# Performance work log

Measured on AMD Instinct MI355X. Metric: run time of the kernel, lower is better.

The kernel has to match this reference:

```python
import jax, jax.numpy as jnp
import numpy as np

GROUPS = 32
EPS = 1e-5

def group_norm(x, scale, bias):
    b, c, h, w = x.shape
    xg = x.reshape(b, GROUPS, c // GROUPS, h, w)
    mean = xg.mean(axis=(2, 3, 4), keepdims=True)
    var = xg.var(axis=(2, 3, 4), keepdims=True)
    xg = (xg - mean) * jax.lax.rsqrt(var + EPS)
    x = xg.reshape(b, c, h, w)
    return x * scale[None, :, None, None] + bias[None, :, None, None]

def conv2d(x, w, b, pad):
    y = jax.lax.conv_general_dilated(
        x, w, window_strides=(1, 1), padding=[(pad, pad), (pad, pad)],
        dimension_numbers=('NCHW', 'OIHW', 'NCHW'))
    return y + b[None, :, None, None]

def setup_inputs() -> dict:
    key = jax.random.key(0)
    ks = jax.random.split(key, 16)
    B, Cin, Cout, H, W, TDIM, NCON = 4, 128, 128, 64, 64, 512, 4
    s = 0.05
    return {
        'x': jax.random.normal(ks[0], (B, Cin, H, W), jnp.float32),
        't': jax.random.normal(ks[1], (B, TDIM), jnp.float32),
        'aim': jax.random.randint(ks[2], (B,), 0, NCON),
        'cond': jax.random.normal(ks[3], (B, Cin, H, W), jnp.float32),
        'gn1_scale': jnp.ones((Cin,), jnp.float32),
        'gn1_bias': jnp.zeros((Cin,), jnp.float32),
        'conv1_w': jax.random.normal(ks[4], (Cout, Cin, 3, 3), jnp.float32) * s,
        'conv1_b': jnp.zeros((Cout,), jnp.float32),
        'mlp_w': jax.random.normal(ks[5], (Cout, TDIM), jnp.float32) * s,
        'mlp_b': jnp.zeros((Cout,), jnp.float32),
        'cond_w': jax.random.normal(ks[6], (Cout, Cin, 1, 1), jnp.float32) * s,
        'cond_b': jnp.zeros((Cout,), jnp.float32),
        'gn2_scale': jnp.ones((Cout,), jnp.float32),
        'gn2_bias': jnp.zeros((Cout,), jnp.float32),
        'conv2_w': jax.random.normal(ks[7], (Cout, Cout, 3, 3), jnp.float32) * s,
        'conv2_b': jnp.zeros((Cout,), jnp.float32),
        'contrast_embed': jax.random.normal(ks[8], (NCON, Cout, 1, 1), jnp.float32),
    }

def reference(x, t, aim, cond, gn1_scale, gn1_bias, conv1_w, conv1_b,
              mlp_w, mlp_b, cond_w, cond_b, gn2_scale, gn2_bias,
              conv2_w, conv2_b, contrast_embed):
    # block1: GN -> SiLU -> 3x3 conv
    h = conv2d(jax.nn.silu(group_norm(x, gn1_scale, gn1_bias)), conv1_w, conv1_b, 1)
    # time embedding: SiLU -> Linear, broadcast over spatial
    temb = jax.nn.silu(t) @ mlp_w.T + mlp_b  # (b, out_ch)
    h = h + temb[:, :, None, None]
    # spatial cross-attention with cond
    c = conv2d(cond, cond_w, cond_b, 0)  # 1x1 projection, (b, C, u, v)
    C = h.shape[1]
    score = jnp.einsum('bchw,bcuv->bhwuv', h, c)  # (b, h, w, u, v)
    # NOTE: softmax over dim=1 (the spatial h axis), as in the source
    score = jax.nn.softmax(score / jnp.sqrt(jnp.float32(C)), axis=1)
    h = h + jnp.einsum('bhwuv,bcuv->bchw', score, c)
    # contrast embedding lookup
    h = h + contrast_embed[aim]  # (b, C, 1, 1) broadcast
    # block2: GN -> SiLU -> (dropout=identity at eval) -> 3x3 conv
    h = conv2d(jax.nn.silu(group_norm(h, gn2_scale, gn2_bias)), conv2_w, conv2_b, 1)
    # res_conv is Identity since in_ch == out_ch
    return h + x
```

## Files before the change

kernel.cpp:

```cpp
#include <hip/hip_runtime.h>
#include <cmath>

#define BB 4
#define CC 128
#define HH 64
#define WW 64
#define SP 4096
#define NG 32
#define TT 64
#define NS 2
#define PSZ ((size_t)BB * SP * CC)

typedef __bf16 bf16x8 __attribute__((ext_vector_type(8)));
typedef __bf16 bf16x4 __attribute__((ext_vector_type(4)));
typedef float  f32x4  __attribute__((ext_vector_type(4)));

__device__ __forceinline__ float silu_f(float v) {
    return v / (1.f + __expf(-v));
}

__device__ __forceinline__ float fast_exp2(float x) {
    return exp2f(x);
}

template<int CTRL>
__device__ __forceinline__ float dpp_add(float v) {
    int m = __builtin_amdgcn_update_dpp(0, __float_as_int(v), CTRL, 0xF, 0xF, true);
    return v + __int_as_float(m);
}
__device__ __forceinline__ float row16_sum(float v) {
    v = dpp_add<0xB1>(v);
    v = dpp_add<0x4E>(v);
    v = dpp_add<0x141>(v);
    v = dpp_add<0x140>(v);
    return v;
}

__global__ __launch_bounds__(256) void prep_kernel(
    const float* __restrict__ x, const float* __restrict__ gn1s,
    const float* __restrict__ gn1b, __bf16* __restrict__ aT,
    const float* __restrict__ c1w, const float* __restrict__ c2w,
    __bf16* __restrict__ wt,
    const float* __restrict__ t, const float* __restrict__ mlpw,
    const float* __restrict__ mlpb, float* __restrict__ tembw,
    const float* __restrict__ cond, const float* __restrict__ cw,
    const float* __restrict__ cb, __bf16* __restrict__ cmT,
    __bf16* __restrict__ cm2)
{
    __shared__ __align__(16) char pool[18432];
    __shared__ float rs[4], rs2[4], mean_s, inv_s;
    const int blk = blockIdx.x;
    const int tid = threadIdx.x;

    if (blk < 128) {
        const int b = blk >> 5, g = blk & 31;
        const float* p = x + (size_t)blk * 16384;
        float s = 0.f, s2 = 0.f;
        for (int it = 0; it < 16; ++it) {
            int q = it * 256 + tid;
            float4 v = *(const float4*)&p[q * 4];
            s += v.x + v.y + v.z + v.w;
            s2 += v.x * v.x + v.y * v.y + v.z * v.z + v.w * v.w;
        }
        #pragma unroll
        for (int off = 32; off >= 1; off >>= 1) {
            s  += __shfl_down(s,  off, 64);
            s2 += __shfl_down(s2, off, 64);
        }
        const int wid = tid >> 6;
        if ((tid & 63) == 0) { rs[wid] = s; rs2[wid] = s2; }
        __syncthreads();
        if (tid == 0) {
            float S = rs[0] + rs[1] + rs[2] + rs[3];
            float S2 = rs2[0] + rs2[1] + rs2[2] + rs2[3];
            float m = S * (1.f / 16384.f);
            float var = S2 * (1.f / 16384.f) - m * m;
            mean_s = m;
            inv_s = rsqrtf(var + 1e-5f);
        }
        __syncthreads();
        const float m = mean_s, inv = inv_s;
        float sc[4], bi[4];
        #pragma unroll
        for (int j = 0; j < 4; ++j) { sc[j] = gn1s[g * 4 + j]; bi[j] = gn1b[g * 4 + j]; }
        for (int it = 0; it < 16; ++it) {
            int pp = it * 256 + tid;
            bf16x4 o;
            #pragma unroll
            for (int j = 0; j < 4; ++j)
                o[j] = (__bf16)silu_f((p[j * 4096 + pp] - m) * inv * sc[j] + bi[j]);
            *(bf16x4*)&aT[((size_t)(b * SP + pp)) * CC + g * 4] = o;
        }
    } else if (blk < 146) {
        const int idx = blk - 128;
        const int wsel = idx / 9, tap = idx % 9;
        const float* src = wsel ? c2w : c1w;
        __bf16* dst = wt + (size_t)wsel * 9 * 16384 + (size_t)tap * 16384;
        for (int it = 0; it < 64; ++it) {
            int q = it * 256 + tid;
            dst[q] = (__bf16)src[(size_t)q * 9 + tap];
        }
    } else if (blk < 154) {
        const int cog = blk - 146;
        float* st = (float*)pool;
        for (int it = 0; it < 8; ++it) {
            int q = it * 256 + tid;
            st[q] = silu_f(t[q]);
        }
        __syncthreads();
        const int col = tid >> 4, seg = tid & 15;
        const float* wr = mlpw + (size_t)(cog * 16 + col) * 512 + seg * 32;
        float acc[4] = {0.f, 0.f, 0.f, 0.f};
        #pragma unroll
        for (int k8 = 0; k8 < 8; ++k8) {
            float4 wv = *(const float4*)&wr[k8 * 4];
            #pragma unroll
            for (int j = 0; j < 4; ++j) {
                int k = seg * 32 + k8 * 4 + j;
                float w4 = (&wv.x)[j];
                acc[0] += st[0 * 512 + k] * w4;
                acc[1] += st[1 * 512 + k] * w4;
                acc[2] += st[2 * 512 + k] * w4;
                acc[3] += st[3 * 512 + k] * w4;
            }
        }
        #pragma unroll
        for (int o = 1; o < 16; o <<= 1) {
            #pragma unroll
            for (int b4 = 0; b4 < 4; ++b4)
                acc[b4] += __shfl_xor(acc[b4], o, 64);
        }
        if (seg == 0) {
            float bv = mlpb[cog * 16 + col];
            #pragma unroll
            for (int b4 = 0; b4 < 4; ++b4)
                tembw[b4 * 128 + cog * 16 + col] = acc[b4] + bv;
        }
    } else {
        const int pblk = blk - 154;
        const int b = pblk >> 6;
        const int p0 = (pblk & 63) * 64;
        const int l = tid & 63, wv = tid >> 6;
        const int l15 = l & 15, l4 = l >> 4;
        const int mB = wv * 32;

        __bf16* XT = (__bf16*)pool;

        for (int it = 0; it < 32; ++it) {
            int q = it * 256 + tid;
            float v = cond[((size_t)(b * CC + (q >> 6))) * SP + p0 + (q & 63)];
            XT[(q & 63) * 136 + (q >> 6)] = (__bf16)v;
        }
        __syncthreads();

        f32x4 acc[2][4];
        #pragma unroll
        for (int mb = 0; mb < 2; ++mb)
            #pragma unroll
            for (int nt = 0; nt < 4; ++nt) acc[mb][nt] = (f32x4){0.f, 0.f, 0.f, 0.f};

        #pragma unroll
        for (int ks = 0; ks < 4; ++ks) {
            bf16x8 bfr[4];
            #pragma unroll
            for (int nt = 0; nt < 4; ++nt)
                bfr[nt] = *(const bf16x8*)&XT[(nt * 16 + l15) * 136 + ks * 32 + l4 * 8];
            #pragma unroll
            for (int mb = 0; mb < 2; ++mb) {
                const float* wrow = cw + (size_t)(mB + mb * 16 + l15) * 128 + ks * 32 + l4 * 8;
                float4 wa = *(const float4*)wrow;
                float4 wb4 = *(const float4*)(wrow + 4);
                bf16x8 afr;
                afr[0] = (__bf16)wa.x; afr[1] = (__bf16)wa.y;
                afr[2] = (__bf16)wa.z; afr[3] = (__bf16)wa.w;
                afr[4] = (__bf16)wb4.x; afr[5] = (__bf16)wb4.y;
                afr[6] = (__bf16)wb4.z; afr[7] = (__bf16)wb4.w;
                #pragma unroll
                for (int nt = 0; nt < 4; ++nt)
                    acc[mb][nt] = __builtin_amdgcn_mfma_f32_16x16x32_bf16(afr, bfr[nt], acc[mb][nt], 0, 0, 0);
            }
        }

        const float scl = 0.12751743f;
        #pragma unroll
        for (int mb = 0; mb < 2; ++mb) {
            int co0 = mB + mb * 16 + l4 * 4;
            float bv[4];
            #pragma unroll
            for (int r = 0; r < 4; ++r) bv[r] = cb[co0 + r];
            #pragma unroll
            for (int nt = 0; nt < 4; ++nt) {
                int p = p0 + nt * 16 + l15;
                bf16x4 o;
                #pragma unroll
                for (int r = 0; r < 4; ++r)
                    o[r] = (__bf16)((acc[mb][nt][r] + bv[r]) * scl);
                *(bf16x4*)&cmT[((size_t)(b * SP + p)) * CC + co0] = o;
            }
        }
        __syncthreads();
        __bf16* O2 = (__bf16*)pool;
        #pragma unroll
        for (int mb = 0; mb < 2; ++mb) {
            int co0 = mB + mb * 16 + l4 * 4;
            #pragma unroll
            for (int r = 0; r < 4; ++r) {
                float bv = cb[co0 + r];
                #pragma unroll
                for (int nt = 0; nt < 4; ++nt)
                    O2[(co0 + r) * 72 + nt * 16 + l15] = (__bf16)(acc[mb][nt][r] + bv);
            }
        }
        __syncthreads();
        #pragma unroll
        for (int it = 0; it < 4; ++it) {
            int q = it * 256 + tid;
            int co = q >> 3, pc = q & 7;
            *(bf16x8*)&cm2[((size_t)(b * CC + co)) * SP + p0 + pc * 8] =
                *(const bf16x8*)&O2[co * 72 + pc * 8];
        }
    }
}

template<bool FUSE_TEMB, bool OUT_CF, bool FUSE_GN>
__global__ __launch_bounds__(256, 4) void conv_mfma_kernel(
    const __bf16* __restrict__ inT, const __bf16* __restrict__ wt,
    const float* __restrict__ bias, const float* __restrict__ temb,
    const float* __restrict__ resid, __bf16* __restrict__ outT,
    float* __restrict__ outF, const float* __restrict__ gstat,
    const float* __restrict__ gn_s, const float* __restrict__ gn_b)
{
    const int y   = blockIdx.x >> 2;
    const int xh2 = (blockIdx.x >> 1) & 1;
    const int coh = blockIdx.x & 1;
    const int x0  = xh2 * 32;
    const int b   = blockIdx.y;
    const int tid = threadIdx.x;
    const int l = tid & 63, wv = tid >> 6;
    const int l15 = l & 15, l4 = l >> 4;
    const int co_w = coh * 64 + wv * 16;

    __shared__ __bf16 inS[3 * 16 * 34 * 8];
    __shared__ float af[128], bfp[128];

    if (FUSE_GN) {
        if (tid < 128) {
            int g = tid >> 2;
            float S = gstat[(b * NG + g) * 2], S2 = gstat[(b * NG + g) * 2 + 1];
            float m = S * (1.f / 16384.f);
            float var = S2 * (1.f / 16384.f) - m * m;
            float inv = rsqrtf(var + 1e-5f);
            float a = inv * gn_s[tid];
            af[tid] = a;
            bfp[tid] = gn_b[tid] - m * a;
        }
        __syncthreads();
    }

    const __bf16* inTb = inT + (size_t)b * SP * CC;
    for (int q = tid; q < 3 * 34 * 16; q += 256) {
        int cc = q & 15;
        int t2 = q >> 4;
        int xs = t2 % 34;
        int r  = t2 / 34;
        int yy = y + r - 1;
        int xg = x0 + xs - 1;
        bf16x8 v;
        if (((unsigned)yy < 64u) && ((unsigned)xg < 64u)) {
            bf16x8 raw = *(const bf16x8*)&inTb[((size_t)(yy * 64 + xg)) * CC + cc * 8];
            if (FUSE_GN) {
                #pragma unroll
                for (int j = 0; j < 8; ++j) {
                    int c = cc * 8 + j;
                    v[j] = (__bf16)silu_f((float)raw[j] * af[c] + bfp[c]);
                }
            } else {
                v = raw;
            }
        } else {
            #pragma unroll
            for (int j = 0; j < 8; ++j) v[j] = (__bf16)0.f;
        }
        *(bf16x8*)&inS[((r * 16 + cc) * 34 + xs) * 8] = v;
    }
    __syncthreads();

    f32x4 acc[2];
    acc[0] = (f32x4){0.f, 0.f, 0.f, 0.f};
    acc[1] = (f32x4){0.f, 0.f, 0.f, 0.f};

    const __bf16* wp = wt + (size_t)(co_w + l15) * 128 + l4 * 8;
    bf16x8 wb[2][4];
    #pragma unroll
    for (int ks = 0; ks < 4; ++ks)
        wb[0][ks] = *(const bf16x8*)(wp + ks * 32);

    #pragma unroll
    for (int tap = 0; tap < 9; ++tap) {
        const int cur = tap & 1, nxt = cur ^ 1;
        if (tap < 8) {
            #pragma unroll
            for (int ks = 0; ks < 4; ++ks)
                wb[nxt][ks] = *(const bf16x8*)(wp + (tap + 1) * 16384 + ks * 32);
        }
        const int rr = tap / 3, dx = tap % 3;
        #pragma unroll
        for (int ks = 0; ks < 4; ++ks) {
            const __bf16* rb = &inS[((rr * 16 + ks * 4 + l4) * 34) * 8];
            bf16x8 b0 = *(const bf16x8*)&rb[(dx + l15) * 8];
            bf16x8 b1 = *(const bf16x8*)&rb[(16 + dx + l15) * 8];
            acc[0] = __builtin_amdgcn_mfma_f32_16x16x32_bf16(wb[cur][ks], b0, acc[0], 0, 0, 0);
            acc[1] = __builtin_amdgcn_mfma_f32_16x16x32_bf16(wb[cur][ks], b1, acc[1], 0, 0, 0);
        }
    }

    if (OUT_CF) {
        #pragma unroll
        for (int r = 0; r < 4; ++r) {
            int co = co_w + l4 * 4 + r;
            float bv = bias[co];
            #pragma unroll
            for (int nb = 0; nb < 2; ++nb) {
                int p = y * 64 + x0 + nb * 16 + l15;
                size_t o = ((size_t)(b * CC + co)) * SP + p;
                outF[o] = acc[nb][r] + bv + resid[o];
            }
        }
    } else {
        int co0 = co_w + l4 * 4;
        float bv[4];
        #pragma unroll
        for (int r = 0; r < 4; ++r)
            bv[r] = bias[co0 + r] + (FUSE_TEMB ? temb[b * CC + co0 + r] : 0.f);
        #pragma unroll
        for (int nb = 0; nb < 2; ++nb) {
            int p = y * 64 + x0 + nb * 16 + l15;
            bf16x4 o;
            #pragma unroll
            for (int r = 0; r < 4; ++r)
                o[r] = (__bf16)(acc[nb][r] + bv[r]);
            *(bf16x4*)&outT[((size_t)(b * SP + p)) * CC + co0] = o;
        }
    }
}

#define CT2 72
#define PBS 72
#define POOL_BYTES 55296

__global__ __launch_bounds__(256, 2) void attn_kernel(
    const __bf16* __restrict__ h1T, const __bf16* __restrict__ cmT,
    const __bf16* __restrict__ cm2, __bf16* __restrict__ parts)
{
    const int w = blockIdx.x;
    const int b = blockIdx.y;
    const int s = blockIdx.z;
    const int tid = threadIdx.x;
    const int wl = tid >> 6;
    const int l = tid & 63, l15 = l & 15, l4 = l >> 4;
    const int hB = (wl & 1) * 32;
    const int cB = (wl >> 1) * 64;

    __shared__ __align__(16) char pool[POOL_BYTES];
    __bf16* ct2p = (__bf16*)pool;
    __bf16* Pbp  = (__bf16*)(pool + 36864);
    __bf16* Otr  = (__bf16*)pool;

    const __bf16* h1Tb = h1T + (size_t)b * SP * CC;
    const __bf16* cmTb = cmT + (size_t)b * SP * CC;
    const __bf16* cm2b = cm2 + (size_t)b * CC * SP;

    bf16x8 hfr[4][4];
    #pragma unroll
    for (int nt = 0; nt < 4; ++nt)
        #pragma unroll
        for (int ks = 0; ks < 4; ++ks)
            hfr[nt][ks] = *(const bf16x8*)&h1Tb[((size_t)((nt * 16 + l15) * WW + w)) * CC + ks * 32 + l4 * 8];

    f32x4 acc2[2][4];
    #pragma unroll
    for (int mb = 0; mb < 2; ++mb)
        #pragma unroll
        for (int nt = 0; nt < 4; ++nt) acc2[mb][nt] = (f32x4){0.f, 0.f, 0.f, 0.f};

    const int sc = tid >> 3;
    const int stc = tid & 7;

    {
        const int uv0 = s * TT;
        #pragma unroll
        for (int it = 0; it < 4; ++it) {
            int c = it * 32 + sc;
            *(bf16x8*)&ct2p[c * CT2 + stc * 8] =
                *(const bf16x8*)&cm2b[(size_t)c * SP + uv0 + stc * 8];
        }
        const __bf16* arow = cmTb + (size_t)(uv0 + 16 * wl + l15) * CC;
        bf16x8 afr[4];
        #pragma unroll
        for (int ks = 0; ks < 4; ++ks) afr[ks] = *(const bf16x8*)&arow[ks * 32 + l4 * 8];
        f32x4 s1[4];
        __builtin_amdgcn_s_setprio(1);
        #pragma unroll
        for (int nt = 0; nt < 4; ++nt) {
            s1[nt] = (f32x4){0.f, 0.f, 0.f, 0.f};
            #pragma unroll
            for (int ks = 0; ks < 4; ++ks)
                s1[nt] = __builtin_amdgcn_mfma_f32_16x16x32_bf16(afr[ks], hfr[nt][ks], s1[nt], 0, 0, 0);
        }
        __builtin_amdgcn_s_setprio(0);
        #pragma unroll
        for (int r = 0; r < 4; ++r) {
            float e0 = fast_exp2(s1[0][r]), e1 = fast_exp2(s1[1][r]);
            float e2 = fast_exp2(s1[2][r]), e3 = fast_exp2(s1[3][r]);
            float sm = (e0 + e1) + (e2 + e3);
            sm = row16_sum(sm);
            float ri = 1.f / sm;
            s1[0][r] = e0 * ri; s1[1][r] = e1 * ri;
            s1[2][r] = e2 * ri; s1[3][r] = e3 * ri;
        }
        #pragma unroll
        for (int nt = 0; nt < 4; ++nt) {
            bf16x4 pk;
            pk[0] = (__bf16)s1[nt][0]; pk[1] = (__bf16)s1[nt][1];
            pk[2] = (__bf16)s1[nt][2]; pk[3] = (__bf16)s1[nt][3];
            *(bf16x4*)&Pbp[(nt * 16 + l15) * PBS + 16 * wl + l4 * 4] = pk;
        }
    }

    for (int i = 0; i < SP / TT / NS; ++i) {
        const int cur = i & 1;
        __syncthreads();
        bf16x8 st4[4];
        bf16x8 afr[4];
        if (i < SP / TT / NS - 1) {
            const int uv0n = ((i + 1) * NS + s) * TT;
            #pragma unroll
            for (int it = 0; it < 4; ++it) {
                int c = it * 32 + sc;
                st4[it] = *(const bf16x8*)&cm2b[(size_t)c * SP + uv0n + stc * 8];
            }
            const __bf16* arow = cmTb + (size_t)(uv0n + 16 * wl + l15) * CC;
            #pragma unroll
            for (int ks = 0; ks < 4; ++ks) afr[ks] = *(const bf16x8*)&arow[ks * 32 + l4 * 8];
        }
        {
            const __bf16* PbR = Pbp + cur * 4608;
            const __bf16* ctR = ct2p + cur * 9216;
            bf16x8 pfr[2][2];
            #pragma unroll
            for (int mb = 0; mb < 2; ++mb)
                #pragma unroll
                for (int ks = 0; ks < 2; ++ks)
                    pfr[mb][ks] = *(const bf16x8*)&PbR[(hB + mb * 16 + l15) * PBS + ks * 32 + l4 * 8];
            bf16x8 bfr[4][2];
            #pragma unroll
            for (int nt = 0; nt < 4; ++nt)
                #pragma unroll
                for (int ks = 0; ks < 2; ++ks)
                    bfr[nt][ks] = *(const bf16x8*)&ctR[(cB + nt * 16 + l15) * CT2 + ks * 32 + l4 * 8];
            __builtin_amdgcn_s_setprio(1);
            #pragma unroll
            for (int mb = 0; mb < 2; ++mb)
                #pragma unroll
                for (int nt = 0; nt < 4; ++nt)
                    #pragma unroll
                    for (int ks = 0; ks < 2; ++ks)
                        acc2[mb][nt] = __builtin_amdgcn_mfma_f32_16x16x32_bf16(
                            pfr[mb][ks], bfr[nt][ks], acc2[mb][nt], 0, 0, 0);
            __builtin_amdgcn_s_setprio(0);
        }
        if (i < SP / TT / NS - 1) {
            __bf16* ctW = ct2p + (cur ^ 1) * 9216;
            #pragma unroll
            for (int it = 0; it < 4; ++it) {
                int c = it * 32 + sc;
                *(bf16x8*)&ctW[c * CT2 + stc * 8] = st4[it];
            }
            f32x4 s1[4];
            __builtin_amdgcn_s_setprio(1);
            #pragma unroll
            for (int nt = 0; nt < 4; ++nt) {
                s1[nt] = (f32x4){0.f, 0.f, 0.f, 0.f};
                #pragma unroll
                for (int ks = 0; ks < 4; ++ks)
                    s1[nt] = __builtin_amdgcn_mfma_f32_16x16x32_bf16(afr[ks], hfr[nt][ks], s1[nt], 0, 0, 0);
            }
            __builtin_amdgcn_s_setprio(0);
            #pragma unroll
            for (int r = 0; r < 4; ++r) {
                float e0 = fast_exp2(s1[0][r]), e1 = fast_exp2(s1[1][r]);
                float e2 = fast_exp2(s1[2][r]), e3 = fast_exp2(s1[3][r]);
                float sm = (e0 + e1) + (e2 + e3);
                sm = row16_sum(sm);
                float ri = 1.f / sm;
                s1[0][r] = e0 * ri; s1[1][r] = e1 * ri;
                s1[2][r] = e2 * ri; s1[3][r] = e3 * ri;
            }
            __bf16* PbW = Pbp + (cur ^ 1) * 4608;
            #pragma unroll
            for (int nt = 0; nt < 4; ++nt) {
                bf16x4 pk;
                pk[0] = (__bf16)s1[nt][0]; pk[1] = (__bf16)s1[nt][1];
                pk[2] = (__bf16)s1[nt][2]; pk[3] = (__bf16)s1[nt][3];
                *(bf16x4*)&PbW[(nt * 16 + l15) * PBS + 16 * wl + l4 * 4] = pk;
            }
        }
    }

    __syncthreads();
    #pragma unroll
    for (int mb = 0; mb < 2; ++mb)
        #pragma unroll
        for (int nt = 0; nt < 4; ++nt)
            #pragma unroll
            for (int r = 0; r < 4; ++r)
                Otr[(hB + mb * 16 + l4 * 4 + r) * 136 + cB + nt * 16 + l15] =
                    (__bf16)acc2[mb][nt][r];
    __syncthreads();
    __bf16* pO = parts + (size_t)s * PSZ;
    #pragma unroll
    for (int it = 0; it < 4; ++it) {
        int q = it * 256 + tid;
        int h = q >> 4, cc = q & 15;
        *(bf16x8*)&pO[((size_t)(b * SP + h * WW + w)) * CC + cc * 8] =
            *(const bf16x8*)&Otr[h * 136 + cc * 8];
    }
}

__global__ __launch_bounds__(256) void gn2_stats_kernel(
    const __bf16* __restrict__ h1T, const __bf16* __restrict__ parts,
    const int* __restrict__ aim, const float* __restrict__ emb,
    __bf16* __restrict__ h2T, float* __restrict__ gstat)
{
    const int pb = blockIdx.x, b = blockIdx.y;
    const int tid = threadIdx.x;
    const int c4 = tid & 31;
    const float4 ev = *(const float4*)&emb[aim[b] * CC + c4 * 4];
    float s = 0.f, s2 = 0.f;
    for (int it = 0; it < 8; ++it) {
        int prow = it * 8 + (tid >> 5);
        size_t base = ((size_t)(b * SP + pb * 64 + prow)) * CC + c4 * 4;
        bf16x4 hv = *(const bf16x4*)&h1T[base];
        float v0 = (float)hv[0] + ev.x;
        float v1 = (float)hv[1] + ev.y;
        float v2 = (float)hv[2] + ev.z;
        float v3 = (float)hv[3] + ev.w;
        #pragma unroll
        for (int k = 0; k < NS; ++k) {
            bf16x4 a = *(const bf16x4*)&parts[(size_t)k * PSZ + base];
            v0 += (float)a[0]; v1 += (float)a[1];
            v2 += (float)a[2]; v3 += (float)a[3];
        }
        bf16x4 o;
        o[0] = (__bf16)v0; o[1] = (__bf16)v1;
        o[2] = (__bf16)v2; o[3] = (__bf16)v3;
        *(bf16x4*)&h2T[base] = o;
        s += v0 + v1 + v2 + v3;
        s2 += v0 * v0 + v1 * v1 + v2 * v2 + v3 * v3;
    }
    s  += __shfl_down(s,  32, 64);
    s2 += __shfl_down(s2, 32, 64);
    __shared__ float ls[4][32][2];
    const int wv = tid >> 6, ll = tid & 63;
    if (ll < 32) { ls[wv][ll][0] = s; ls[wv][ll][1] = s2; }
    __syncthreads();
    if (tid < 32) {
        float S = ls[0][tid][0] + ls[1][tid][0] + ls[2][tid][0] + ls[3][tid][0];
        float S2 = ls[0][tid][1] + ls[1][tid][1] + ls[2][tid][1] + ls[3][tid][1];
        atomicAdd(&gstat[(b * NG + tid) * 2], S);
        atomicAdd(&gstat[(b * NG + tid) * 2 + 1], S2);
    }
}

extern "C" void kernel_launch(void* const* d_in, const int* in_sizes, int n_in,
                              void* d_out, int out_size, void* d_ws, size_t ws_size,
                              hipStream_t stream)
{
    const float* x     = (const float*)d_in[0];
    const float* t     = (const float*)d_in[1];
    const int*   aim   = (const int*)  d_in[2];
    const float* cond  = (const float*)d_in[3];
    const float* gn1s  = (const float*)d_in[4];
    const float* gn1b  = (const float*)d_in[5];
    const float* c1w   = (const float*)d_in[6];
    const float* c1b   = (const float*)d_in[7];
    const float* mlpw  = (const float*)d_in[8];
    const float* mlpb  = (const float*)d_in[9];
    const float* cw    = (const float*)d_in[10];
    const float* cb    = (const float*)d_in[11];
    const float* gn2s  = (const float*)d_in[12];
    const float* gn2b  = (const float*)d_in[13];
    const float* c2w   = (const float*)d_in[14];
    const float* c2b   = (const float*)d_in[15];
    const float* emb   = (const float*)d_in[16];
    float* out = (float*)d_out;
    float* ws = (float*)d_ws;

    __bf16* aT    = (__bf16*)ws;
    __bf16* h1T   = (__bf16*)(ws + 1048576);
    __bf16* cmT   = (__bf16*)(ws + 2097152);
    __bf16* cm2   = (__bf16*)(ws + 3145728);
    __bf16* parts = (__bf16*)(ws + 4194304);
    __bf16* wt    = (__bf16*)(ws + 6291456);
    float*  tembw = ws + 6438912;
    float*  gstat = ws + 6439424;
    __bf16* h2T   = cmT;

    prep_kernel<<<dim3(410), dim3(256), 0, stream>>>(
        x, gn1s, gn1b, aT, c1w, c2w, wt, t, mlpw, mlpb, tembw,
        cond, cw, cb, cmT, cm2);
    hipMemsetAsync(gstat, 0, 256 * sizeof(float), stream);
    conv_mfma_kernel<true, false, false><<<dim3(256, BB), dim3(256), 0, stream>>>(
        aT, wt, c1b, tembw, nullptr, h1T, nullptr, nullptr, nullptr, nullptr);
    attn_kernel<<<dim3(WW, BB, NS), dim3(256), 0, stream>>>(h1T, cmT, cm2, parts);
    gn2_stats_kernel<<<dim3(64, BB), dim3(256), 0, stream>>>(h1T, parts, aim, emb, h2T, gstat);
    conv_mfma_kernel<false, true, true><<<dim3(256, BB), dim3(256), 0, stream>>>(
        h2T, wt + (size_t)9 * 16384, c2b, nullptr, x, nullptr, out, gstat, gn2s, gn2b);
}
```

Before: 222.9 us.

## Split attention key range four ways and single-buffer cond tile to raise occupancy

Doubles the split of the attention key/uv dimension from 2 to 4 so the grid has twice as many blocks, each doing half the iterations. The cond tile in shared memory goes from double- to single-buffered, with an extra barrier before the next tile is written, which cuts LDS use and allows 4 blocks per CU. The two extra partial outputs reuse the aT workspace and the output buffer as scratch, and gn2_stats now sums four partials. This costs more partial-sum traffic and one more sync per iteration, with less overlap of shared-memory writes and compute.

```diff
diff --git a/kernel.cpp b/kernel.cpp
--- a/kernel.cpp
+++ b/kernel.cpp
@@ -8,7 +8,7 @@
 #define SP 4096
 #define NG 32
 #define TT 64
-#define NS 2
+#define NS 4
 #define PSZ ((size_t)BB * SP * CC)
 
 typedef __bf16 bf16x8 __attribute__((ext_vector_type(8)));
@@ -346,11 +346,13 @@
 
 #define CT2 72
 #define PBS 72
-#define POOL_BYTES 55296
-
-__global__ __launch_bounds__(256, 2) void attn_kernel(
+#define POOL_BYTES 36864
+
+__global__ __launch_bounds__(256, 4) void attn_kernel(
     const __bf16* __restrict__ h1T, const __bf16* __restrict__ cmT,
-    const __bf16* __restrict__ cm2, __bf16* __restrict__ parts)
+    const __bf16* __restrict__ cm2,
+    __bf16* __restrict__ pp0, __bf16* __restrict__ pp1,
+    __bf16* __restrict__ pp2, __bf16* __restrict__ pp3)
 {
     const int w = blockIdx.x;
     const int b = blockIdx.y;
@@ -363,7 +365,7 @@
 
     __shared__ __align__(16) char pool[POOL_BYTES];
     __bf16* ct2p = (__bf16*)pool;
-    __bf16* Pbp  = (__bf16*)(pool + 36864);
+    __bf16* Pbp  = (__bf16*)(pool + 18432);
     __bf16* Otr  = (__bf16*)pool;
 
     const __bf16* h1Tb = h1T + (size_t)b * SP * CC;
@@ -427,12 +429,13 @@
         }
     }
 
-    for (int i = 0; i < SP / TT / NS; ++i) {
+    const int NIT = SP / TT / NS;
+    for (int i = 0; i < NIT; ++i) {
         const int cur = i & 1;
         __syncthreads();
         bf16x8 st4[4];
         bf16x8 afr[4];
-        if (i < SP / TT / NS - 1) {
+        if (i < NIT - 1) {
             const int uv0n = ((i + 1) * NS + s) * TT;
             #pragma unroll
             for (int it = 0; it < 4; ++it) {
@@ -445,7 +448,6 @@
         }
         {
             const __bf16* PbR = Pbp + cur * 4608;
-            const __bf16* ctR = ct2p + cur * 9216;
             bf16x8 pfr[2][2];
             #pragma unroll
             for (int mb = 0; mb < 2; ++mb)
@@ -457,7 +459,7 @@
             for (int nt = 0; nt < 4; ++nt)
                 #pragma unroll
                 for (int ks = 0; ks < 2; ++ks)
-                    bfr[nt][ks] = *(const bf16x8*)&ctR[(cB + nt * 16 + l15) * CT2 + ks * 32 + l4 * 8];
+                    bfr[nt][ks] = *(const bf16x8*)&ct2p[(cB + nt * 16 + l15) * CT2 + ks * 32 + l4 * 8];
             __builtin_amdgcn_s_setprio(1);
             #pragma unroll
             for (int mb = 0; mb < 2; ++mb)
@@ -469,13 +471,7 @@
                             pfr[mb][ks], bfr[nt][ks], acc2[mb][nt], 0, 0, 0);
             __builtin_amdgcn_s_setprio(0);
         }
-        if (i < SP / TT / NS - 1) {
-            __bf16* ctW = ct2p + (cur ^ 1) * 9216;
-            #pragma unroll
-            for (int it = 0; it < 4; ++it) {
-                int c = it * 32 + sc;
-                *(bf16x8*)&ctW[c * CT2 + stc * 8] = st4[it];
-            }
+        if (i < NIT - 1) {
             f32x4 s1[4];
             __builtin_amdgcn_s_setprio(1);
             #pragma unroll
@@ -505,6 +501,14 @@
                 *(bf16x4*)&PbW[(nt * 16 + l15) * PBS + 16 * wl + l4 * 4] = pk;
             }
         }
+        __syncthreads();
+        if (i < NIT - 1) {
+            #pragma unroll
+            for (int it = 0; it < 4; ++it) {
+                int c = it * 32 + sc;
+                *(bf16x8*)&ct2p[c * CT2 + stc * 8] = st4[it];
+            }
+        }
     }
 
     __syncthreads();
@@ -517,7 +521,7 @@
                 Otr[(hB + mb * 16 + l4 * 4 + r) * 136 + cB + nt * 16 + l15] =
                     (__bf16)acc2[mb][nt][r];
     __syncthreads();
-    __bf16* pO = parts + (size_t)s * PSZ;
+    __bf16* pO = (s == 0) ? pp0 : (s == 1) ? pp1 : (s == 2) ? pp2 : pp3;
     #pragma unroll
     for (int it = 0; it < 4; ++it) {
         int q = it * 256 + tid;
@@ -528,7 +532,9 @@
 }
 
 __global__ __launch_bounds__(256) void gn2_stats_kernel(
-    const __bf16* __restrict__ h1T, const __bf16* __restrict__ parts,
+    const __bf16* __restrict__ h1T,
+    const __bf16* __restrict__ pp0, const __bf16* __restrict__ pp1,
+    const __bf16* __restrict__ pp2, const __bf16* __restrict__ pp3,
     const int* __restrict__ aim, const float* __restrict__ emb,
     __bf16* __restrict__ h2T, float* __restrict__ gstat)
 {
@@ -545,12 +551,14 @@
         float v1 = (float)hv[1] + ev.y;
         float v2 = (float)hv[2] + ev.z;
         float v3 = (float)hv[3] + ev.w;
-        #pragma unroll
-        for (int k = 0; k < NS; ++k) {
-            bf16x4 a = *(const bf16x4*)&parts[(size_t)k * PSZ + base];
-            v0 += (float)a[0]; v1 += (float)a[1];
-            v2 += (float)a[2]; v3 += (float)a[3];
-        }
+        bf16x4 a0 = *(const bf16x4*)&pp0[base];
+        bf16x4 a1 = *(const bf16x4*)&pp1[base];
+        bf16x4 a2 = *(const bf16x4*)&pp2[base];
+        bf16x4 a3 = *(const bf16x4*)&pp3[base];
+        v0 += (float)a0[0] + (float)a1[0] + (float)a2[0] + (float)a3[0];
+        v1 += (float)a0[1] + (float)a1[1] + (float)a2[1] + (float)a3[1];
+        v2 += (float)a0[2] + (float)a1[2] + (float)a2[2] + (float)a3[2];
+        v3 += (float)a0[3] + (float)a1[3] + (float)a2[3] + (float)a3[3];
         bf16x4 o;
         o[0] = (__bf16)v0; o[1] = (__bf16)v1;
         o[2] = (__bf16)v2; o[3] = (__bf16)v3;
@@ -605,6 +613,8 @@
     float*  tembw = ws + 6438912;
     float*  gstat = ws + 6439424;
     __bf16* h2T   = cmT;
+    __bf16* part2 = aT;
+    __bf16* part3 = (__bf16*)out;
 
     prep_kernel<<<dim3(410), dim3(256), 0, stream>>>(
         x, gn1s, gn1b, aT, c1w, c2w, wt, t, mlpw, mlpb, tembw,
@@ -612,8 +622,10 @@
     hipMemsetAsync(gstat, 0, 256 * sizeof(float), stream);
     conv_mfma_kernel<true, false, false><<<dim3(256, BB), dim3(256), 0, stream>>>(
         aT, wt, c1b, tembw, nullptr, h1T, nullptr, nullptr, nullptr, nullptr);
-    attn_kernel<<<dim3(WW, BB, NS), dim3(256), 0, stream>>>(h1T, cmT, cm2, parts);
-    gn2_stats_kernel<<<dim3(64, BB), dim3(256), 0, stream>>>(h1T, parts, aim, emb, h2T, gstat);
+    attn_kernel<<<dim3(WW, BB, NS), dim3(256), 0, stream>>>(
+        h1T, cmT, cm2, parts, parts + PSZ, part2, part3);
+    gn2_stats_kernel<<<dim3(64, BB), dim3(256), 0, stream>>>(
+        h1T, parts, parts + PSZ, part2, part3, aim, emb, h2T, gstat);
     conv_mfma_kernel<false, true, true><<<dim3(256, BB), dim3(256), 0, stream>>>(
         h2T, wt + (size_t)9 * 16384, c2b, nullptr, x, nullptr, out, gstat, gn2s, gn2b);
 }
```

Result: slower. 335.4 us (+50.5%).

## Split attention kernel into producer softmax waves and consumer PV waves

Applied to the files above, without the earlier changes.

The attention kernel grows to 512 threads and specializes its waves. Four waves compute the QK scores, the exp2 softmax and the P tiles into double-buffered LDS. The other four waves stream the cond tiles and run the P·V MFMAs, so the two stages overlap across the barrier instead of running back to back in the same waves. The launch bound of (512,4) sharply limits registers per thread, while the producer alone holds 64 VGPRs of h fragments, so register spills are a real risk; LDS size also limits how many blocks fit per CU.

```diff
diff --git a/kernel.cpp b/kernel.cpp
--- a/kernel.cpp
+++ b/kernel.cpp
@@ -347,8 +347,9 @@
 #define CT2 72
 #define PBS 72
 #define POOL_BYTES 55296
-
-__global__ __launch_bounds__(256, 2) void attn_kernel(
+#define NIT (SP / TT / NS)
+
+__global__ __launch_bounds__(512, 4) void attn_kernel(
     const __bf16* __restrict__ h1T, const __bf16* __restrict__ cmT,
     const __bf16* __restrict__ cm2, __bf16* __restrict__ parts)
 {
@@ -356,10 +357,8 @@
     const int b = blockIdx.y;
     const int s = blockIdx.z;
     const int tid = threadIdx.x;
-    const int wl = tid >> 6;
+    const int wid = tid >> 6;
     const int l = tid & 63, l15 = l & 15, l4 = l >> 4;
-    const int hB = (wl & 1) * 32;
-    const int cB = (wl >> 1) * 64;
 
     __shared__ __align__(16) char pool[POOL_BYTES];
     __bf16* ct2p = (__bf16*)pool;
@@ -370,112 +369,21 @@
     const __bf16* cmTb = cmT + (size_t)b * SP * CC;
     const __bf16* cm2b = cm2 + (size_t)b * CC * SP;
 
-    bf16x8 hfr[4][4];
-    #pragma unroll
-    for (int nt = 0; nt < 4; ++nt)
-        #pragma unroll
-        for (int ks = 0; ks < 4; ++ks)
-            hfr[nt][ks] = *(const bf16x8*)&h1Tb[((size_t)((nt * 16 + l15) * WW + w)) * CC + ks * 32 + l4 * 8];
-
-    f32x4 acc2[2][4];
-    #pragma unroll
-    for (int mb = 0; mb < 2; ++mb)
-        #pragma unroll
-        for (int nt = 0; nt < 4; ++nt) acc2[mb][nt] = (f32x4){0.f, 0.f, 0.f, 0.f};
-
-    const int sc = tid >> 3;
-    const int stc = tid & 7;
-
-    {
-        const int uv0 = s * TT;
-        #pragma unroll
-        for (int it = 0; it < 4; ++it) {
-            int c = it * 32 + sc;
-            *(bf16x8*)&ct2p[c * CT2 + stc * 8] =
-                *(const bf16x8*)&cm2b[(size_t)c * SP + uv0 + stc * 8];
-        }
-        const __bf16* arow = cmTb + (size_t)(uv0 + 16 * wl + l15) * CC;
-        bf16x8 afr[4];
-        #pragma unroll
-        for (int ks = 0; ks < 4; ++ks) afr[ks] = *(const bf16x8*)&arow[ks * 32 + l4 * 8];
-        f32x4 s1[4];
-        __builtin_amdgcn_s_setprio(1);
-        #pragma unroll
-        for (int nt = 0; nt < 4; ++nt) {
-            s1[nt] = (f32x4){0.f, 0.f, 0.f, 0.f};
+    if (wid < 4) {
+        const int pw = wid;
+        bf16x8 hfr[4][4];
+        #pragma unroll
+        for (int nt = 0; nt < 4; ++nt)
             #pragma unroll
             for (int ks = 0; ks < 4; ++ks)
-                s1[nt] = __builtin_amdgcn_mfma_f32_16x16x32_bf16(afr[ks], hfr[nt][ks], s1[nt], 0, 0, 0);
-        }
-        __builtin_amdgcn_s_setprio(0);
-        #pragma unroll
-        for (int r = 0; r < 4; ++r) {
-            float e0 = fast_exp2(s1[0][r]), e1 = fast_exp2(s1[1][r]);
-            float e2 = fast_exp2(s1[2][r]), e3 = fast_exp2(s1[3][r]);
-            float sm = (e0 + e1) + (e2 + e3);
-            sm = row16_sum(sm);
-            float ri = 1.f / sm;
-            s1[0][r] = e0 * ri; s1[1][r] = e1 * ri;
-            s1[2][r] = e2 * ri; s1[3][r] = e3 * ri;
-        }
-        #pragma unroll
-        for (int nt = 0; nt < 4; ++nt) {
-            bf16x4 pk;
-            pk[0] = (__bf16)s1[nt][0]; pk[1] = (__bf16)s1[nt][1];
-            pk[2] = (__bf16)s1[nt][2]; pk[3] = (__bf16)s1[nt][3];
-            *(bf16x4*)&Pbp[(nt * 16 + l15) * PBS + 16 * wl + l4 * 4] = pk;
-        }
-    }
-
-    for (int i = 0; i < SP / TT / NS; ++i) {
-        const int cur = i & 1;
-        __syncthreads();
-        bf16x8 st4[4];
-        bf16x8 afr[4];
-        if (i < SP / TT / NS - 1) {
-            const int uv0n = ((i + 1) * NS + s) * TT;
-            #pragma unroll
-            for (int it = 0; it < 4; ++it) {
-                int c = it * 32 + sc;
-                st4[it] = *(const bf16x8*)&cm2b[(size_t)c * SP + uv0n + stc * 8];
-            }
-            const __bf16* arow = cmTb + (size_t)(uv0n + 16 * wl + l15) * CC;
+                hfr[nt][ks] = *(const bf16x8*)&h1Tb[((size_t)((nt * 16 + l15) * WW + w)) * CC + ks * 32 + l4 * 8];
+
+        {
+            const int uv0 = s * TT;
+            const __bf16* arow = cmTb + (size_t)(uv0 + 16 * pw + l15) * CC;
+            bf16x8 afr[4];
             #pragma unroll
             for (int ks = 0; ks < 4; ++ks) afr[ks] = *(const bf16x8*)&arow[ks * 32 + l4 * 8];
-        }
-        {
-            const __bf16* PbR = Pbp + cur * 4608;
-            const __bf16* ctR = ct2p + cur * 9216;
-            bf16x8 pfr[2][2];
-            #pragma unroll
-            for (int mb = 0; mb < 2; ++mb)
-                #pragma unroll
-                for (int ks = 0; ks < 2; ++ks)
-                    pfr[mb][ks] = *(const bf16x8*)&PbR[(hB + mb * 16 + l15) * PBS + ks * 32 + l4 * 8];
-            bf16x8 bfr[4][2];
-            #pragma unroll
-            for (int nt = 0; nt < 4; ++nt)
-                #pragma unroll
-                for (int ks = 0; ks < 2; ++ks)
-                    bfr[nt][ks] = *(const bf16x8*)&ctR[(cB + nt * 16 + l15) * CT2 + ks * 32 + l4 * 8];
-            __builtin_amdgcn_s_setprio(1);
-            #pragma unroll
-            for (int mb = 0; mb < 2; ++mb)
-                #pragma unroll
-                for (int nt = 0; nt < 4; ++nt)
-                    #pragma unroll
-                    for (int ks = 0; ks < 2; ++ks)
-                        acc2[mb][nt] = __builtin_amdgcn_mfma_f32_16x16x32_bf16(
-                            pfr[mb][ks], bfr[nt][ks], acc2[mb][nt], 0, 0, 0);
-            __builtin_amdgcn_s_setprio(0);
-        }
-        if (i < SP / TT / NS - 1) {
-            __bf16* ctW = ct2p + (cur ^ 1) * 9216;
-            #pragma unroll
-            for (int it = 0; it < 4; ++it) {
-                int c = it * 32 + sc;
-                *(bf16x8*)&ctW[c * CT2 + stc * 8] = st4[it];
-            }
             f32x4 s1[4];
             __builtin_amdgcn_s_setprio(1);
             #pragma unroll
@@ -496,31 +404,142 @@
                 s1[0][r] = e0 * ri; s1[1][r] = e1 * ri;
                 s1[2][r] = e2 * ri; s1[3][r] = e3 * ri;
             }
-            __bf16* PbW = Pbp + (cur ^ 1) * 4608;
             #pragma unroll
             for (int nt = 0; nt < 4; ++nt) {
                 bf16x4 pk;
                 pk[0] = (__bf16)s1[nt][0]; pk[1] = (__bf16)s1[nt][1];
                 pk[2] = (__bf16)s1[nt][2]; pk[3] = (__bf16)s1[nt][3];
-                *(bf16x4*)&PbW[(nt * 16 + l15) * PBS + 16 * wl + l4 * 4] = pk;
-            }
-        }
-    }
-
-    __syncthreads();
-    #pragma unroll
-    for (int mb = 0; mb < 2; ++mb)
-        #pragma unroll
-        for (int nt = 0; nt < 4; ++nt)
-            #pragma unroll
-            for (int r = 0; r < 4; ++r)
-                Otr[(hB + mb * 16 + l4 * 4 + r) * 136 + cB + nt * 16 + l15] =
-                    (__bf16)acc2[mb][nt][r];
+                *(bf16x4*)&Pbp[(nt * 16 + l15) * PBS + 16 * pw + l4 * 4] = pk;
+            }
+        }
+        __syncthreads();
+
+        for (int i = 0; i < NIT; ++i) {
+            if (i < NIT - 1) {
+                const int uv0n = ((i + 1) * NS + s) * TT;
+                const __bf16* arow = cmTb + (size_t)(uv0n + 16 * pw + l15) * CC;
+                bf16x8 afr[4];
+                #pragma unroll
+                for (int ks = 0; ks < 4; ++ks) afr[ks] = *(const bf16x8*)&arow[ks * 32 + l4 * 8];
+                f32x4 s1[4];
+                __builtin_amdgcn_s_setprio(1);
+                #pragma unroll
+                for (int nt = 0; nt < 4; ++nt) {
+                    s1[nt] = (f32x4){0.f, 0.f, 0.f, 0.f};
+                    #pragma unroll
+                    for (int ks = 0; ks < 4; ++ks)
+                        s1[nt] = __builtin_amdgcn_mfma_f32_16x16x32_bf16(afr[ks], hfr[nt][ks], s1[nt], 0, 0, 0);
+                }
+                __builtin_amdgcn_s_setprio(0);
+                #pragma unroll
+                for (int r = 0; r < 4; ++r) {
+                    float e0 = fast_exp2(s1[0][r]), e1 = fast_exp2(s1[1][r]);
+                    float e2 = fast_exp2(s1[2][r]), e3 = fast_exp2(s1[3][r]);
+                    float sm = (e0 + e1) + (e2 + e3);
+                    sm = row16_sum(sm);
+                    float ri = 1.f / sm;
+                    s1[0][r] = e0 * ri; s1[1][r] = e1 * ri;
+                    s1[2][r] = e2 * ri; s1[3][r] = e3 * ri;
+                }
+                __bf16* PbW = Pbp + ((i & 1) ^ 1) * 4608;
+                #pragma unroll
+                for (int nt = 0; nt < 4; ++nt) {
+                    bf16x4 pk;
+                    pk[0] = (__bf16)s1[nt][0]; pk[1] = (__bf16)s1[nt][1];
+                    pk[2] = (__bf16)s1[nt][2]; pk[3] = (__bf16)s1[nt][3];
+                    *(bf16x4*)&PbW[(nt * 16 + l15) * PBS + 16 * pw + l4 * 4] = pk;
+                }
+            }
+            __syncthreads();
+        }
+    } else {
+        const int cw = wid - 4;
+        const int hB = (cw & 1) * 32;
+        const int cB = (cw >> 1) * 64;
+        const int tc = tid - 256;
+        const int sc = tc >> 3;
+        const int stc = tc & 7;
+
+        f32x4 acc2[2][4];
+        #pragma unroll
+        for (int mb = 0; mb < 2; ++mb)
+            #pragma unroll
+            for (int nt = 0; nt < 4; ++nt) acc2[mb][nt] = (f32x4){0.f, 0.f, 0.f, 0.f};
+
+        {
+            const int uv0 = s * TT;
+            #pragma unroll
+            for (int it = 0; it < 4; ++it) {
+                int c = it * 32 + sc;
+                *(bf16x8*)&ct2p[c * CT2 + stc * 8] =
+                    *(const bf16x8*)&cm2b[(size_t)c * SP + uv0 + stc * 8];
+            }
+        }
+        __syncthreads();
+
+        for (int i = 0; i < NIT; ++i) {
+            const int cur = i & 1;
+            bf16x8 st4[4];
+            if (i < NIT - 1) {
+                const int uv0n = ((i + 1) * NS + s) * TT;
+                #pragma unroll
+                for (int it = 0; it < 4; ++it) {
+                    int c = it * 32 + sc;
+                    st4[it] = *(const bf16x8*)&cm2b[(size_t)c * SP + uv0n + stc * 8];
+                }
+            }
+            {
+                const __bf16* PbR = Pbp + cur * 4608;
+                const __bf16* ctR = ct2p + cur * 9216;
+                bf16x8 pfr[2][2];
+                #pragma unroll
+                for (int mb = 0; mb < 2; ++mb)
+                    #pragma unroll
+                    for (int ks = 0; ks < 2; ++ks)
+                        pfr[mb][ks] = *(const bf16x8*)&PbR[(hB + mb * 16 + l15) * PBS + ks * 32 + l4 * 8];
+                bf16x8 bfr[4][2];
+                #pragma unroll
+                for (int nt = 0; nt < 4; ++nt)
+                    #pragma unroll
+                    for (int ks = 0; ks < 2; ++ks)
+                        bfr[nt][ks] = *(const bf16x8*)&ctR[(cB + nt * 16 + l15) * CT2 + ks * 32 + l4 * 8];
+                __builtin_amdgcn_s_setprio(1);
+                #pragma unroll
+                for (int mb = 0; mb < 2; ++mb)
+                    #pragma unroll
+                    for (int nt = 0; nt < 4; ++nt)
+                        #pragma unroll
+                        for (int ks = 0; ks < 2; ++ks)
+                            acc2[mb][nt] = __builtin_amdgcn_mfma_f32_16x16x32_bf16(
+                                pfr[mb][ks], bfr[nt][ks], acc2[mb][nt], 0, 0, 0);
+                __builtin_amdgcn_s_setprio(0);
+            }
+            if (i < NIT - 1) {
+                __bf16* ctW = ct2p + (cur ^ 1) * 9216;
+                #pragma unroll
+                for (int it = 0; it < 4; ++it) {
+                    int c = it * 32 + sc;
+                    *(bf16x8*)&ctW[c * CT2 + stc * 8] = st4[it];
+                }
+            }
+            __syncthreads();
+        }
+
+        #pragma unroll
+        for (int mb = 0; mb < 2; ++mb)
+            #pragma unroll
+            for (int nt = 0; nt < 4; ++nt)
+                #pragma unroll
+                for (int r = 0; r < 4; ++r)
+                    Otr[(hB + mb * 16 + l4 * 4 + r) * 136 + cB + nt * 16 + l15] =
+                        (__bf16)acc2[mb][nt][r];
+    }
+
     __syncthreads();
     __bf16* pO = parts + (size_t)s * PSZ;
     #pragma unroll
-    for (int it = 0; it < 4; ++it) {
-        int q = it * 256 + tid;
+    for (int it = 0; it < 2; ++it) {
+        int q = it * 512 + tid;
         int h = q >> 4, cc = q & 15;
         *(bf16x8*)&pO[((size_t)(b * SP + h * WW + w)) * CC + cc * 8] =
             *(const bf16x8*)&Otr[h * 136 + cc * 8];
@@ -612,7 +631,7 @@
     hipMemsetAsync(gstat, 0, 256 * sizeof(float), stream);
     conv_mfma_kernel<true, false, false><<<dim3(256, BB), dim3(256), 0, stream>>>(
         aT, wt, c1b, tembw, nullptr, h1T, nullptr, nullptr, nullptr, nullptr);
-    attn_kernel<<<dim3(WW, BB, NS), dim3(256), 0, stream>>>(h1T, cmT, cm2, parts);
+    attn_kernel<<<dim3(WW, BB, NS), dim3(512), 0, stream>>>(h1T, cmT, cm2, parts);
     gn2_stats_kernel<<<dim3(64, BB), dim3(256), 0, stream>>>(h1T, parts, aim, emb, h2T, gstat);
     conv_mfma_kernel<false, true, true><<<dim3(256, BB), dim3(256), 0, stream>>>(
         h2T, wt + (size_t)9 * 16384, c2b, nullptr, x, nullptr, out, gstat, gn2s, gn2b);
```

Measured after the change: 220.5 us. About the same (-1.1%).
